# Kernel optimization log

Measured on AMD Instinct MI355X. Metric: run time of the kernel, lower is better.

Reference implementation:

```python
import jax, jax.numpy as jnp
import numpy as np

N_S, N_T, E = 50000, 50000, 600000
D_IN, D_H, D_OUT = 256, 128, 64


def setup_inputs() -> dict:
    key = jax.random.key(0)
    k1, k2, k3, k4, k5, k6 = jax.random.split(key, 6)
    edge_src = jax.random.randint(k1, (E,), 0, N_S, dtype=jnp.int32)
    edge_dst = jax.random.randint(k2, (E,), 0, N_T, dtype=jnp.int32)
    edge_index = jnp.stack([edge_src, edge_dst], axis=0)  # [2, E]
    x_s = jax.random.normal(k3, (N_S, D_IN), dtype=jnp.float32)
    x_t = jax.random.normal(k4, (N_T, D_IN), dtype=jnp.float32)
    W0 = jax.random.normal(k5, (D_IN, D_H), dtype=jnp.float32) * (1.0 / np.sqrt(D_IN))
    W1 = jax.random.normal(k6, (D_H, D_OUT), dtype=jnp.float32) * (1.0 / np.sqrt(D_H))
    return {"edge_index": edge_index, "x_s": x_s, "x_t": x_t, "W0": W0, "W1": W1}


def gcn_conv(x, src, dst, W):
    """PyG GCNConv, bias=False: D^{-1/2}(A+I)D^{-1/2} (x @ W)."""
    N = x.shape[0]
    h = x @ W  # [N, out]
    loops = jnp.arange(N, dtype=src.dtype)
    s = jnp.concatenate([src, loops])  # add self-loops
    d = jnp.concatenate([dst, loops])
    deg = jax.ops.segment_sum(jnp.ones_like(d, dtype=h.dtype), d, num_segments=N)
    dinv = jnp.where(deg > 0, jax.lax.rsqrt(deg), 0.0)
    norm = dinv[s] * dinv[d]  # [E+N]
    return jax.ops.segment_sum(h[s] * norm[:, None], d, num_segments=N)


def reference(edge_index, x_s, x_t, W0, W1):
    n_s = x_s.shape[0]
    src = edge_index[0]
    dst = edge_index[1] + n_s  # targets live in the x_t block
    acts = [jax.nn.relu, lambda v: v]
    Ws = [W0, W1]
    for W, act in zip(Ws, acts):
        x = jnp.concatenate([x_s, x_t], axis=0)
        x = act(gcn_conv(x, src, dst, W))
        x_s, x_t = x[:n_s], x[n_s:]
    return (x_s, x_t)
```

## Files before the change

### kernel.cpp

```cpp
#include <hip/hip_runtime.h>
#include <cstdint>
#include <cstddef>

typedef unsigned short u16;
typedef unsigned int   u32;
typedef __attribute__((ext_vector_type(8))) short bf16x8;
typedef __attribute__((ext_vector_type(4))) float f32x4;

#define D_IN  256
#define D_H   128
#define D_OUT 64

__device__ __forceinline__ float bf2f(u16 u){
  union { u32 i; float f; } v; v.i = ((u32)u) << 16; return v.f;
}
__device__ __forceinline__ u16 f2bf(float f){
  union { float f; u32 i; } v; v.f = f;
  u32 r = (v.i + 0x7fffu + ((v.i >> 16) & 1u)) >> 16;
  return (u16)r;
}

__global__ void k_wprep(const float* __restrict__ W0, const float* __restrict__ W1,
                        u16* __restrict__ W0t, u16* __restrict__ W1t,
                        int* __restrict__ deg, int n_t){
  int i = blockIdx.x * 256 + threadIdx.x;
  if (i < 128 * 256){
    int n = i >> 8, k = i & 255;
    W0t[i] = f2bf(W0[(size_t)k * 128 + n]);
  } else if (i < 128 * 256 + 64 * 128){
    int j = i - 128 * 256;
    int n = j >> 7, k = j & 127;
    W1t[j] = f2bf(W1[(size_t)k * 64 + n]);
  } else if (i - (128 * 256 + 64 * 128) < n_t){
    deg[i - (128 * 256 + 64 * 128)] = 0;
  }
}

__global__ void k_deg(const int* __restrict__ dst, int E, int* __restrict__ deg){
  int e = blockIdx.x * 256 + threadIdx.x;
  if (e < E) atomicAdd(&deg[dst[e]], 1);
}

__global__ __launch_bounds__(256) void k_bsum(const int* __restrict__ deg, int N,
                                              int* __restrict__ bsum){
  __shared__ int s[256];
  int tid = threadIdx.x;
  int i = blockIdx.x * 256 + tid;
  s[tid] = (i < N) ? deg[i] : 0;
  __syncthreads();
  for (int o = 128; o > 0; o >>= 1){
    if (tid < o) s[tid] += s[tid + o];
    __syncthreads();
  }
  if (tid == 0) bsum[blockIdx.x] = s[0];
}

__global__ __launch_bounds__(256) void k_off(const int* __restrict__ deg, int N,
                                             const int* __restrict__ bsum, int nb,
                                             int* __restrict__ off, int* __restrict__ cursor,
                                             float* __restrict__ dinv){
  __shared__ int s[256];
  __shared__ int sbase[256];
  const int tid = threadIdx.x;
  const int bid = blockIdx.x;
  const int i   = bid * 256 + tid;
  int acc = 0;
  for (int j = tid; j < bid; j += 256) acc += bsum[j];
  sbase[tid] = acc;
  int v = (i < N) ? deg[i] : 0;
  s[tid] = v;
  __syncthreads();
  for (int o = 128; o > 0; o >>= 1){
    if (tid < o) sbase[tid] += sbase[tid + o];
    __syncthreads();
  }
  for (int o = 1; o < 256; o <<= 1){
    int t = (tid >= o) ? s[tid - o] : 0;
    __syncthreads();
    s[tid] += t;
    __syncthreads();
  }
  if (i < N){
    int excl = s[tid] - v + sbase[0];
    off[i] = excl;
    cursor[i] = excl;
    dinv[i] = rsqrtf((float)v + 1.0f);
  }
}

__global__ void k_fill(const int* __restrict__ src, const int* __restrict__ dst,
                       int E, int* __restrict__ cursor, int* __restrict__ csr){
  int e = blockIdx.x * 256 + threadIdx.x;
  if (e < E){
    int d = dst[e];
    int p = atomicAdd(&cursor[d], 1);
    csr[p] = src[e];
  }
}

__global__ __launch_bounds__(256) void k_gemm1(
    const float* __restrict__ Xs, const float* __restrict__ Xt,
    const u16* __restrict__ W0t, int M, int n_s,
    u16* __restrict__ out)
{
  const int t    = threadIdx.x;
  const int wave = t >> 6, lane = t & 63;
  const int lm   = lane & 15, quad = lane >> 4;
  const int rowW = blockIdx.x * 128 + wave * 32;

  const float* pa0;
  const float* pa1;
  {
    int r0 = rowW + lm;       int c0 = (r0 < M) ? r0 : 0;
    int r1 = rowW + 16 + lm;  int c1 = (r1 < M) ? r1 : 0;
    pa0 = ((c0 < n_s) ? (Xs + (size_t)c0 * D_IN) : (Xt + (size_t)(c0 - n_s) * D_IN)) + quad * 8;
    pa1 = ((c1 < n_s) ? (Xs + (size_t)c1 * D_IN) : (Xt + (size_t)(c1 - n_s) * D_IN)) + quad * 8;
  }
  const u16* pb = W0t + (size_t)lm * D_IN + quad * 8;

  f32x4 acc[2][8];
  const f32x4 z = {0.f, 0.f, 0.f, 0.f};
  #pragma unroll
  for (int i = 0; i < 2; i++)
    #pragma unroll
    for (int j = 0; j < 8; j++) acc[i][j] = z;

  float4 a[2][4];
  int4   b[2][8];

  a[0][0] = *(const float4*)(pa0);
  a[0][1] = *(const float4*)(pa0 + 4);
  a[0][2] = *(const float4*)(pa1);
  a[0][3] = *(const float4*)(pa1 + 4);
  #pragma unroll
  for (int nf = 0; nf < 8; nf++)
    b[0][nf] = *(const int4*)(pb + (size_t)nf * 16 * D_IN);

  #pragma unroll
  for (int kk = 0; kk < 8; kk++){
    const int cur = kk & 1, nxt = cur ^ 1;
    if (kk < 7){
      const int ko = (kk + 1) * 32;
      a[nxt][0] = *(const float4*)(pa0 + ko);
      a[nxt][1] = *(const float4*)(pa0 + ko + 4);
      a[nxt][2] = *(const float4*)(pa1 + ko);
      a[nxt][3] = *(const float4*)(pa1 + ko + 4);
      #pragma unroll
      for (int nf = 0; nf < 8; nf++)
        b[nxt][nf] = *(const int4*)(pb + (size_t)nf * 16 * D_IN + ko);
    }
    bf16x8 af[2];
    #pragma unroll
    for (int mi = 0; mi < 2; mi++){
      const float* fa = (const float*)&a[cur][mi * 2];
      u16 tmp[8];
      #pragma unroll
      for (int q = 0; q < 8; q++) tmp[q] = f2bf(fa[q]);
      af[mi] = *(const bf16x8*)tmp;
    }
    #pragma unroll
    for (int mi = 0; mi < 2; mi++)
      #pragma unroll
      for (int nf = 0; nf < 8; nf++)
        acc[mi][nf] = __builtin_amdgcn_mfma_f32_16x16x32_bf16(
            af[mi], *(const bf16x8*)&b[cur][nf], acc[mi][nf], 0, 0, 0);
  }

  #pragma unroll
  for (int mi = 0; mi < 2; mi++){
    int rbase = rowW + mi * 16 + quad * 4;
    #pragma unroll
    for (int rr = 0; rr < 4; rr++){
      int m = rbase + rr;
      if (m >= M) continue;
      u16* op = out + (size_t)m * D_H + lm;
      #pragma unroll
      for (int nf = 0; nf < 8; nf++)
        op[nf * 16] = f2bf(acc[mi][nf][rr]);
    }
  }
}

__global__ __launch_bounds__(256) void k_aggf(
    const int* __restrict__ off, const int* __restrict__ deg,
    const int* __restrict__ csr, const float* __restrict__ dinv,
    u16* __restrict__ h1, int n_s, int n_t)
{
  int w    = (blockIdx.x * 256 + threadIdx.x) >> 6;
  int lane = threadIdx.x & 63;
  if (w >= n_t) return;
  const int g = lane >> 4;
  const int c = lane & 15;
  int start = off[w];
  int n     = deg[w];

  float r[8], p[8];
  #pragma unroll
  for (int q = 0; q < 8; q++){ r[q] = 0.f; p[q] = 0.f; }

  int i = 0;
  for (; i + 8 <= n; i += 8){
    int sa = csr[start + i + g];
    int sb = csr[start + i + 4 + g];
    int4 da = *(const int4*)(h1 + (size_t)sa * D_H + c * 8);
    int4 db = *(const int4*)(h1 + (size_t)sb * D_H + c * 8);
    const u16* ha = (const u16*)&da;
    const u16* hb = (const u16*)&db;
    #pragma unroll
    for (int q = 0; q < 8; q++){
      float va = bf2f(ha[q]), vb = bf2f(hb[q]);
      r[q] += va + vb;
      p[q] += fmaxf(va, 0.f) + fmaxf(vb, 0.f);
    }
  }
  for (; i < n; i += 4){
    if (i + g < n){
      int sa = csr[start + i + g];
      int4 da = *(const int4*)(h1 + (size_t)sa * D_H + c * 8);
      const u16* ha = (const u16*)&da;
      #pragma unroll
      for (int q = 0; q < 8; q++){
        float va = bf2f(ha[q]);
        r[q] += va;
        p[q] += fmaxf(va, 0.f);
      }
    }
  }

  #pragma unroll
  for (int q = 0; q < 8; q++){
    r[q] += __shfl_xor(r[q], 16, 64);
    r[q] += __shfl_xor(r[q], 32, 64);
    p[q] += __shfl_xor(p[q], 16, 64);
    p[q] += __shfl_xor(p[q], 32, 64);
  }

  if (g == 0){
    float di  = dinv[w];
    float di2 = di * di;
    u16* selfp = h1 + (size_t)(n_s + w) * D_H + c * 8;
    int4 hs = *(const int4*)selfp;
    const u16* hh = (const u16*)&hs;
    u16 ob[8];
    #pragma unroll
    for (int q = 0; q < 8; q++){
      float zq = fmaxf(di * r[q] + di2 * bf2f(hh[q]), 0.f);
      float uq = di * p[q] + di2 * zq;
      ob[q] = f2bf(uq);
    }
    *(int4*)selfp = *(int4*)ob;
  }
}

__device__ __forceinline__ bf16x8 relu_bf(int4 v, bool relu){
  const u16* s = (const u16*)&v;
  u16 tmp[8];
  #pragma unroll
  for (int q = 0; q < 8; q++){
    u16 x = s[q];
    tmp[q] = (relu && (x & 0x8000u)) ? (u16)0 : x;
  }
  return *(const bf16x8*)tmp;
}

__global__ __launch_bounds__(256) void k_gemm2(
    const u16* __restrict__ h1, const u16* __restrict__ W1t,
    int M, int n_s, float* __restrict__ out)
{
  const int t    = threadIdx.x;
  const int wave = t >> 6, lane = t & 63;
  const int lm   = lane & 15, quad = lane >> 4;
  const int rowW = blockIdx.x * 128 + wave * 32;

  int r0 = rowW + lm, r1 = rowW + 16 + lm;
  const bool relu0 = (r0 < n_s), relu1 = (r1 < n_s);
  int c0 = (r0 < M) ? r0 : 0, c1 = (r1 < M) ? r1 : 0;
  const u16* pa0 = h1 + (size_t)c0 * D_H + quad * 8;
  const u16* pa1 = h1 + (size_t)c1 * D_H + quad * 8;
  const u16* pb  = W1t + (size_t)lm * D_H + quad * 8;

  f32x4 acc[2][4];
  const f32x4 z = {0.f, 0.f, 0.f, 0.f};
  #pragma unroll
  for (int i = 0; i < 2; i++)
    #pragma unroll
    for (int j = 0; j < 4; j++) acc[i][j] = z;

  int4 a[2][2], b[2][4];
  a[0][0] = *(const int4*)(pa0);
  a[0][1] = *(const int4*)(pa1);
  #pragma unroll
  for (int nf = 0; nf < 4; nf++)
    b[0][nf] = *(const int4*)(pb + (size_t)nf * 16 * D_H);

  #pragma unroll
  for (int kk = 0; kk < 4; kk++){
    const int cur = kk & 1, nxt = cur ^ 1;
    if (kk < 3){
      const int ko = (kk + 1) * 32;
      a[nxt][0] = *(const int4*)(pa0 + ko);
      a[nxt][1] = *(const int4*)(pa1 + ko);
      #pragma unroll
      for (int nf = 0; nf < 4; nf++)
        b[nxt][nf] = *(const int4*)(pb + (size_t)nf * 16 * D_H + ko);
    }
    bf16x8 af[2];
    af[0] = relu_bf(a[cur][0], relu0);
    af[1] = relu_bf(a[cur][1], relu1);
    #pragma unroll
    for (int mi = 0; mi < 2; mi++)
      #pragma unroll
      for (int nf = 0; nf < 4; nf++)
        acc[mi][nf] = __builtin_amdgcn_mfma_f32_16x16x32_bf16(
            af[mi], *(const bf16x8*)&b[cur][nf], acc[mi][nf], 0, 0, 0);
  }

  #pragma unroll
  for (int mi = 0; mi < 2; mi++){
    int rbase = rowW + mi * 16 + quad * 4;
    #pragma unroll
    for (int rr = 0; rr < 4; rr++){
      int m = rbase + rr;
      if (m >= M) continue;
      float* op = out + (size_t)m * D_OUT + lm;
      #pragma unroll
      for (int nf = 0; nf < 4; nf++)
        op[nf * 16] = acc[mi][nf][rr];
    }
  }
}

static inline size_t alup(size_t x){ return (x + 255) & ~(size_t)255; }

extern "C" void kernel_launch(void* const* d_in, const int* in_sizes, int n_in,
                              void* d_out, int out_size, void* d_ws, size_t ws_size,
                              hipStream_t stream)
{
  const int*   ei = (const int*)d_in[0];
  const float* xs = (const float*)d_in[1];
  const float* xt = (const float*)d_in[2];
  const float* W0 = (const float*)d_in[3];
  const float* W1 = (const float*)d_in[4];
  const int E   = in_sizes[0] / 2;
  const int n_s = in_sizes[1] / D_IN;
  const int n_t = in_sizes[2] / D_IN;
  const int M   = n_s + n_t;
  const int* src = ei;
  const int* dst = ei + E;
  const int nb_t = (n_t + 255) / 256;

  char* p = (char*)d_ws;
  int*   deg    = (int*)p;    p += alup((size_t)n_t * 4);
  int*   off    = (int*)p;    p += alup((size_t)n_t * 4);
  int*   cursor = (int*)p;    p += alup((size_t)n_t * 4);
  float* dinv   = (float*)p;  p += alup((size_t)n_t * 4);
  int*   bsum   = (int*)p;    p += alup((size_t)nb_t * 4);
  int*   csr    = (int*)p;    p += alup((size_t)E * 4);
  u16*   W0t    = (u16*)p;    p += alup((size_t)D_H * D_IN * 2);
  u16*   W1t    = (u16*)p;    p += alup((size_t)D_OUT * D_H * 2);
  u16*   h1     = (u16*)p;    p += alup((size_t)M * D_H * 2);

  const int wprep_n = 128*256 + 64*128 + n_t;
  k_wprep <<<(wprep_n + 255) / 256, 256, 0, stream>>>(W0, W1, W0t, W1t, deg, n_t);
  k_deg   <<<(E + 255) / 256, 256, 0, stream>>>(dst, E, deg);
  k_bsum  <<<nb_t, 256, 0, stream>>>(deg, n_t, bsum);
  k_off   <<<nb_t, 256, 0, stream>>>(deg, n_t, bsum, nb_t, off, cursor, dinv);
  k_fill  <<<(E + 255) / 256, 256, 0, stream>>>(src, dst, E, cursor, csr);

  k_gemm1<<<(M + 127) / 128, 256, 0, stream>>>(xs, xt, W0t, M, n_s, h1);
  k_aggf <<<(n_t + 3) / 4, 256, 0, stream>>>(off, deg, csr, dinv, h1, n_s, n_t);
  k_gemm2<<<(M + 127) / 128, 256, 0, stream>>>(h1, W1t, M, n_s, (float*)d_out);
}
```

Baseline: 280.6 us.

## Stage GEMM1 A tile through swizzled LDS with coalesced loads

```diff
diff --git a/kernel.cpp b/kernel.cpp
--- a/kernel.cpp
+++ b/kernel.cpp
@@ -103,72 +103,68 @@
     const u16* __restrict__ W0t, int M, int n_s,
     u16* __restrict__ out)
 {
+  __shared__ u16 As[64 * 256];
   const int t    = threadIdx.x;
   const int wave = t >> 6, lane = t & 63;
   const int lm   = lane & 15, quad = lane >> 4;
-  const int rowW = blockIdx.x * 128 + wave * 32;
-
-  const float* pa0;
-  const float* pa1;
+  const int row0 = blockIdx.x * 64;
+
   {
-    int r0 = rowW + lm;       int c0 = (r0 < M) ? r0 : 0;
-    int r1 = rowW + 16 + lm;  int c1 = (r1 < M) ? r1 : 0;
-    pa0 = ((c0 < n_s) ? (Xs + (size_t)c0 * D_IN) : (Xt + (size_t)(c0 - n_s) * D_IN)) + quad * 8;
-    pa1 = ((c1 < n_s) ? (Xs + (size_t)c1 * D_IN) : (Xt + (size_t)(c1 - n_s) * D_IN)) + quad * 8;
-  }
+    float4 st[16];
+    #pragma unroll
+    for (int i = 0; i < 16; i++){
+      int r = row0 + wave + i * 4;
+      const float* p;
+      if (r < n_s)    p = Xs + (size_t)r * D_IN + lane * 4;
+      else if (r < M) p = Xt + (size_t)(r - n_s) * D_IN + lane * 4;
+      else            p = Xs + lane * 4;
+      st[i] = *(const float4*)p;
+    }
+    #pragma unroll
+    for (int i = 0; i < 16; i++){
+      int r = wave + i * 4;
+      u16 tmp[4];
+      tmp[0] = f2bf(st[i].x); tmp[1] = f2bf(st[i].y);
+      tmp[2] = f2bf(st[i].z); tmp[3] = f2bf(st[i].w);
+      int c = (lane * 4) ^ ((r & 7) << 3);
+      *(int2*)&As[r * 256 + c] = *(const int2*)tmp;
+    }
+  }
+  __syncthreads();
+
+  f32x4 acc[8];
+  const f32x4 z = {0.f, 0.f, 0.f, 0.f};
+  #pragma unroll
+  for (int nf = 0; nf < 8; nf++) acc[nf] = z;
+
   const u16* pb = W0t + (size_t)lm * D_IN + quad * 8;
-
-  f32x4 acc[2][8];
-  const f32x4 z = {0.f, 0.f, 0.f, 0.f};
-  #pragma unroll
-  for (int i = 0; i < 2; i++)
-    #pragma unroll
-    for (int j = 0; j < 8; j++) acc[i][j] = z;
-
-  float4 a[2][4];
-  int4   b[2][8];
-
-  a[0][0] = *(const float4*)(pa0);
-  a[0][1] = *(const float4*)(pa0 + 4);
-  a[0][2] = *(const float4*)(pa1);
-  a[0][3] = *(const float4*)(pa1 + 4);
+  int4 b[2][8];
   #pragma unroll
   for (int nf = 0; nf < 8; nf++)
     b[0][nf] = *(const int4*)(pb + (size_t)nf * 16 * D_IN);
+
+  const int ra  = wave * 16 + lm;
+  const int rsw = (ra & 7) << 3;
+  const u16* arow = As + ra * 256;
 
   #pragma unroll
   for (int kk = 0; kk < 8; kk++){
     const int cur = kk & 1, nxt = cur ^ 1;
     if (kk < 7){
       const int ko = (kk + 1) * 32;
-      a[nxt][0] = *(const float4*)(pa0 + ko);
-      a[nxt][1] = *(const float4*)(pa0 + ko + 4);
-      a[nxt][2] = *(const float4*)(pa1 + ko);
-      a[nxt][3] = *(const float4*)(pa1 + ko + 4);
       #pragma unroll
       for (int nf = 0; nf < 8; nf++)
         b[nxt][nf] = *(const int4*)(pb + (size_t)nf * 16 * D_IN + ko);
     }
-    bf16x8 af[2];
-    #pragma unroll
-    for (int mi = 0; mi < 2; mi++){
-      const float* fa = (const float*)&a[cur][mi * 2];
-      u16 tmp[8];
-      #pragma unroll
-      for (int q = 0; q < 8; q++) tmp[q] = f2bf(fa[q]);
-      af[mi] = *(const bf16x8*)tmp;
-    }
-    #pragma unroll
-    for (int mi = 0; mi < 2; mi++)
-      #pragma unroll
-      for (int nf = 0; nf < 8; nf++)
-        acc[mi][nf] = __builtin_amdgcn_mfma_f32_16x16x32_bf16(
-            af[mi], *(const bf16x8*)&b[cur][nf], acc[mi][nf], 0, 0, 0);
-  }
-
-  #pragma unroll
-  for (int mi = 0; mi < 2; mi++){
-    int rbase = rowW + mi * 16 + quad * 4;
+    bf16x8 af = *(const bf16x8*)(arow + ((kk * 32 + quad * 8) ^ rsw));
+    #pragma unroll
+    for (int nf = 0; nf < 8; nf++)
+      acc[nf] = __builtin_amdgcn_mfma_f32_16x16x32_bf16(
+          af, *(const bf16x8*)&b[cur][nf], acc[nf], 0, 0, 0);
+  }
+
+  {
+    int rbase = row0 + wave * 16 + quad * 4;
     #pragma unroll
     for (int rr = 0; rr < 4; rr++){
       int m = rbase + rr;
@@ -176,7 +172,7 @@
       u16* op = out + (size_t)m * D_H + lm;
       #pragma unroll
       for (int nf = 0; nf < 8; nf++)
-        op[nf * 16] = f2bf(acc[mi][nf][rr]);
+        op[nf * 16] = f2bf(acc[nf][rr]);
     }
   }
 }
@@ -367,7 +363,7 @@
   k_off   <<<nb_t, 256, 0, stream>>>(deg, n_t, bsum, nb_t, off, cursor, dinv);
   k_fill  <<<(E + 255) / 256, 256, 0, stream>>>(src, dst, E, cursor, csr);
 
-  k_gemm1<<<(M + 127) / 128, 256, 0, stream>>>(xs, xt, W0t, M, n_s, h1);
+  k_gemm1<<<(M + 63) / 64, 256, 0, stream>>>(xs, xt, W0t, M, n_s, h1);
   k_aggf <<<(n_t + 3) / 4, 256, 0, stream>>>(off, deg, csr, dinv, h1, n_s, n_t);
   k_gemm2<<<(M + 127) / 128, 256, 0, stream>>>(h1, W1t, M, n_s, (float*)d_out);
 }
```

After: 292.1 us. 4.1% more time.
